# Optimization experiments

Measured on AMD Instinct MI355X. Metric: run time of the kernel, lower is better.

## Reference

```python
import jax, jax.numpy as jnp
import numpy as np

B, T, C = 4, 2048, 768
N_HEADS = 16
HEAD_DIM = C // N_HEADS  # 48
ROPE_BASE = 10000.0


def setup_inputs() -> dict:
    key = jax.random.key(0)
    ks = jax.random.split(key, 6)
    s = 0.02
    return {
        "hidden_states": jax.random.normal(ks[0], (B, T, C), dtype=jnp.float32),
        "attention_mask": jnp.ones((B, T), dtype=jnp.float32),
        "Wq": jax.random.normal(ks[1], (C, C), dtype=jnp.float32) * s,
        "bq": jnp.zeros((C,), dtype=jnp.float32),
        "Wk": jax.random.normal(ks[2], (C, C), dtype=jnp.float32) * s,
        "bk": jnp.zeros((C,), dtype=jnp.float32),
        "Wv": jax.random.normal(ks[3], (C, C), dtype=jnp.float32) * s,
        "bv": jnp.zeros((C,), dtype=jnp.float32),
        "Wo": jax.random.normal(ks[4], (C, C), dtype=jnp.float32) * s,
        "bo": jnp.zeros((C,), dtype=jnp.float32),
    }


def _rotate_half(x):
    x1, x2 = jnp.split(x, 2, axis=-1)
    return jnp.concatenate([-x2, x1], axis=-1)


def reference(hidden_states, attention_mask, Wq, bq, Wk, bk, Wv, bv, Wo, bo):
    b, t, c = hidden_states.shape
    h, d = N_HEADS, c // N_HEADS

    def split_heads(x):  # [b,t,c] -> [b,h,t,d]
        return x.reshape(b, t, h, d).transpose(0, 2, 1, 3)

    q = split_heads(hidden_states @ Wq.T + bq)
    k = split_heads(hidden_states @ Wk.T + bk)
    v = split_heads(hidden_states @ Wv.T + bv)

    # rotary embedding: cos/sin [t, d]
    pos = jnp.arange(t, dtype=jnp.float32)
    inv_freq = 1.0 / (ROPE_BASE ** (jnp.arange(0, d, 2, dtype=jnp.float32) / d))
    freqs = pos[:, None] * inv_freq[None, :]          # [t, d/2]
    emb = jnp.concatenate([freqs, freqs], axis=-1)    # [t, d]
    cos, sin = jnp.cos(emb), jnp.sin(emb)
    q = q * cos + _rotate_half(q) * sin
    k = k * cos + _rotate_half(k) * sin

    scores = jnp.einsum('bhqd,bhkd->bhqk', q, k) / jnp.sqrt(jnp.asarray(d, q.dtype))
    # additive padding mask: (1 - mask) * -10000, broadcast [b,1,1,t]
    scores = scores + (1.0 - attention_mask)[:, None, None, :] * -10000.0
    # causal mask with -inf
    causal = jnp.tril(jnp.ones((t, t), dtype=bool))
    scores = jnp.where(causal[None, None], scores, -jnp.inf)

    probs = jax.nn.softmax(scores, axis=-1)
    ctx = jnp.einsum('bhqk,bhkd->bhqd', probs, v)
    ctx = ctx.transpose(0, 2, 1, 3).reshape(b, t, c)
    return ctx @ Wo.T + bo
```

## Files before the change

kernel.cpp:

```cpp
#include <hip/hip_runtime.h>
#include <hip/hip_bf16.h>
#include <math.h>

#define BB 4
#define TT 2048
#define CC 768
#define NHD 16
#define HD 48
#define NQT 32

typedef __hip_bfloat16 bf16;
typedef __attribute__((ext_vector_type(8))) short short8;
typedef __attribute__((ext_vector_type(4))) float floatx4;

__device__ __forceinline__ unsigned short f2bf(float x) {
    bf16 h = __float2bfloat16(x);
    return *(unsigned short*)&h;
}
__device__ __forceinline__ float bfu2f(unsigned short u) {
    return __uint_as_float(((unsigned)u) << 16);
}

__device__ __forceinline__ void gl_lds16(const void* g, void* s) {
    __builtin_amdgcn_global_load_lds((const __attribute__((address_space(1))) void*)g,
                                     (__attribute__((address_space(3))) void*)s, 16, 0, 0);
}

__device__ __forceinline__ unsigned int pk_bf2(float a, float b) {
    unsigned int ua = __float_as_uint(a) + 0x8000u;
    unsigned int ub = __float_as_uint(b) + 0x8000u;
    return __builtin_amdgcn_perm(ub, ua, 0x07060302);
}

__global__ __launch_bounds__(256) void cast_hs(const float* __restrict__ src,
                                               unsigned short* __restrict__ dst) {
    int i = (blockIdx.x * 256 + threadIdx.x) * 4;
    float4 v = *(const float4*)(src + i);
    ushort4 p;
    p.x = f2bf(v.x); p.y = f2bf(v.y); p.z = f2bf(v.z); p.w = f2bf(v.w);
    *(ushort4*)(dst + i) = p;
}

__global__ __launch_bounds__(256) void cast_w4(const float* __restrict__ s0, const float* __restrict__ s1,
                                               const float* __restrict__ s2, const float* __restrict__ s3,
                                               unsigned short* __restrict__ d0, unsigned short* __restrict__ d1,
                                               unsigned short* __restrict__ d2, unsigned short* __restrict__ d3) {
    const float* s; unsigned short* d;
    switch (blockIdx.y) {
        case 0: s = s0; d = d0; break;
        case 1: s = s1; d = d1; break;
        case 2: s = s2; d = d2; break;
        default: s = s3; d = d3; break;
    }
    int i = (blockIdx.x * 256 + threadIdx.x) * 4;
    float4 v = *(const float4*)(s + i);
    ushort4 p;
    p.x = f2bf(v.x); p.y = f2bf(v.y); p.z = f2bf(v.z); p.w = f2bf(v.w);
    *(ushort4*)(d + i) = p;
}

template <int MODE>
__global__ __launch_bounds__(256) void gemm_mfma(const unsigned short* __restrict__ A,
                                                 const unsigned short* __restrict__ Bw,
                                                 const float* __restrict__ b0p,
                                                 const float* __restrict__ b1p,
                                                 const float* __restrict__ b2p,
                                                 void* __restrict__ out0,
                                                 void* __restrict__ out1,
                                                 void* __restrict__ out2) {
    __shared__ __align__(16) unsigned short As[128][64];
    __shared__ __align__(16) unsigned short Bs[128][64];
    const int tid = threadIdx.x;
    const int w = tid >> 6, lane = tid & 63;
    const int quad = lane >> 4, ln = lane & 15;
    const int wr = w >> 1, wc = w & 1;
    const int n0 = blockIdx.x * 128;
    const int m0 = blockIdx.y * 128;

    const int srow = lane >> 3;
    const int ssw = ((lane & 7) ^ srow) * 8;
    const unsigned short* agp[4];
    const unsigned short* bgp[4];
    void* asl[4];
    void* bsl[4];
#pragma unroll
    for (int i = 0; i < 4; ++i) {
        const int R = i * 32 + w * 8;
        agp[i] = A + (size_t)(m0 + R + srow) * CC + ssw;
        bgp[i] = Bw + (size_t)(n0 + R + srow) * CC + ssw;
        asl[i] = &As[R][0];
        bsl[i] = &Bs[R][0];
    }

    floatx4 acc[4][4];
#pragma unroll
    for (int mi = 0; mi < 4; ++mi)
#pragma unroll
        for (int ni = 0; ni < 4; ++ni) acc[mi][ni] = (floatx4){0.f, 0.f, 0.f, 0.f};

    const int ps0 = (quad ^ (ln & 7)) * 8;

    for (int k0 = 0; k0 < CC; k0 += 64) {
        __syncthreads();
#pragma unroll
        for (int i = 0; i < 4; ++i) {
            gl_lds16(agp[i] + k0, asl[i]);
            gl_lds16(bgp[i] + k0, bsl[i]);
        }
        __syncthreads();
#pragma unroll
        for (int kh = 0; kh < 2; ++kh) {
            const int ps = ps0 ^ (kh * 32);
            short8 af[4], bfr[4];
#pragma unroll
            for (int mi = 0; mi < 4; ++mi)
                af[mi] = *(const short8*)&As[wr * 64 + mi * 16 + ln][ps];
#pragma unroll
            for (int ni = 0; ni < 4; ++ni)
                bfr[ni] = *(const short8*)&Bs[wc * 64 + ni * 16 + ln][ps];
#pragma unroll
            for (int mi = 0; mi < 4; ++mi)
#pragma unroll
                for (int ni = 0; ni < 4; ++ni)
                    acc[mi][ni] = __builtin_amdgcn_mfma_f32_16x16x32_bf16(af[mi], bfr[ni], acc[mi][ni], 0, 0, 0);
        }
    }

    if (MODE == 0) {
        float* outf = (float*)out0;
        float bv[4];
#pragma unroll
        for (int ni = 0; ni < 4; ++ni) bv[ni] = b0p[n0 + wc * 64 + ni * 16 + ln];
#pragma unroll
        for (int mi = 0; mi < 4; ++mi)
#pragma unroll
            for (int r = 0; r < 4; ++r) {
                size_t row = m0 + wr * 64 + mi * 16 + quad * 4 + r;
#pragma unroll
                for (int ni = 0; ni < 4; ++ni)
                    outf[row * CC + n0 + wc * 64 + ni * 16 + ln] = acc[mi][ni][r] + bv[ni];
            }
    } else {
        const int seg = n0 / CC;
        const int nl0 = n0 - seg * CC;
        const float* bp = (seg == 0) ? b0p : (seg == 1) ? b1p : b2p;
        float bv[4];
#pragma unroll
        for (int ni = 0; ni < 4; ++ni) bv[ni] = bp[nl0 + wc * 64 + ni * 16 + ln];

        if (seg < 2) {
            unsigned short* outb = (unsigned short*)(seg == 0 ? out0 : out1);
#pragma unroll
            for (int mi = 0; mi < 4; ++mi)
#pragma unroll
                for (int r = 0; r < 4; ++r) {
                    size_t row = m0 + wr * 64 + mi * 16 + quad * 4 + r;
#pragma unroll
                    for (int ni = 0; ni < 4; ++ni)
                        outb[row * CC + nl0 + wc * 64 + ni * 16 + ln] = f2bf(acc[mi][ni][r] + bv[ni]);
                }
        } else {
            unsigned short* outb = (unsigned short*)out2;
            const int b = m0 >> 11;
#pragma unroll
            for (int ni = 0; ni < 4; ++ni) {
                int col = nl0 + wc * 64 + ni * 16 + ln;
                int h = col / HD, d = col % HD;
                size_t base = (size_t)((b * NHD + h) * HD + d) * TT;
#pragma unroll
                for (int mi = 0; mi < 4; ++mi) {
                    int t = (m0 & 2047) + wr * 64 + mi * 16 + quad * 4;
                    ushort4 pk;
                    pk.x = f2bf(acc[mi][ni][0] + bv[ni]);
                    pk.y = f2bf(acc[mi][ni][1] + bv[ni]);
                    pk.z = f2bf(acc[mi][ni][2] + bv[ni]);
                    pk.w = f2bf(acc[mi][ni][3] + bv[ni]);
                    *(ushort4*)(outb + base + t) = pk;
                }
            }
        }
    }
}

__global__ __launch_bounds__(256) void rope_bf(unsigned short* __restrict__ q,
                                               unsigned short* __restrict__ k) {
    int idx = blockIdx.x * blockDim.x + threadIdx.x;
    const int HALF = HD / 2;
    int p = idx % HALF;
    int rest = idx / HALF;
    int h = rest % NHD;
    int n = rest / NHD;
    int t = n % TT;
    const float QSC = 0.14433756729740643f * 1.4426950408889634f;
    float inv_freq = powf(10000.0f, -((float)(2 * p) / (float)HD));
    float ang = (float)t * inv_freq;
    float sn, cs;
    sincosf(ang, &sn, &cs);
    size_t base = (size_t)n * CC + h * HD + p;
    float x1 = bfu2f(q[base]), x2 = bfu2f(q[base + HALF]);
    q[base] = f2bf((x1 * cs - x2 * sn) * QSC);
    q[base + HALF] = f2bf((x2 * cs + x1 * sn) * QSC);
    x1 = bfu2f(k[base]); x2 = bfu2f(k[base + HALF]);
    k[base] = f2bf(x1 * cs - x2 * sn);
    k[base + HALF] = f2bf(x2 * cs + x1 * sn);
}

__global__ __launch_bounds__(256) void attn_kernel(const unsigned short* __restrict__ qb,
                                                   const unsigned short* __restrict__ kb,
                                                   const unsigned short* __restrict__ vt,
                                                   const float* __restrict__ amask,
                                                   unsigned short* __restrict__ ctx) {
    const int pair = blockIdx.x, h = blockIdx.y, b = blockIdx.z;
    const int tid = threadIdx.x;
    const int w = tid >> 6, lane = tid & 63;
    const int g = lane >> 4, ln = lane & 15;

    __shared__ __align__(16) unsigned short Qs[64][72];
    __shared__ __align__(16) unsigned short Ks[64][72];
    __shared__ __align__(16) unsigned short Vs[64][72];
    __shared__ __align__(16) unsigned short Pw[4][16][72];
    __shared__ __align__(16) float l_s[4][16];

    {
        short8 z8 = {0, 0, 0, 0, 0, 0, 0, 0};
        short8 o8 = {0x3F80, 0, 0, 0, 0, 0, 0, 0};
        short8 ones8 = {0x3F80, 0x3F80, 0x3F80, 0x3F80, 0x3F80, 0x3F80, 0x3F80, 0x3F80};
        if (tid < 128) {
            int r = tid >> 1, half = tid & 1;
            *(short8*)&Qs[r][48 + half * 8] = half ? z8 : o8;
            int t2 = tid;
            *(short8*)&Ks[t2 >> 1][48 + (t2 & 1) * 8] = z8;
        } else if (tid < 128 + 144) {
            int t3 = tid - 128;
            int r = 48 + t3 / 9, cseg = t3 % 9;
            *(short8*)&Vs[r][cseg * 8] = (r == 48) ? ones8 : z8;
        }
    }

    const int ck1 = tid + 256;
    const int rK0 = tid / 6, sK0 = tid % 6;
    const int rK1 = ck1 / 6, sK1 = ck1 % 6;
    const int rV0 = tid >> 3, sV0 = tid & 7;
    const int rV1 = ck1 >> 3, sV1 = ck1 & 7;
    const unsigned short* kbase0 = kb + (size_t)(b * TT + rK0) * CC + h * HD + sK0 * 8;
    const unsigned short* kbase1 = kb + (size_t)(b * TT + rK1) * CC + h * HD + sK1 * 8;
    const unsigned short* vbase0 = vt + (size_t)((b * NHD + h) * HD + rV0) * TT + sV0 * 8;
    const unsigned short* vbase1 = vt + (size_t)((b * NHD + h) * HD + rV1) * TT + sV1 * 8;
    const float* mbase = amask + b * TT + (tid & 63);
    const float MBS = -10000.0f * 1.4426950408889634f;

    for (int rep = 0; rep < 2; ++rep) {
        const int qt = rep ? (NQT - 1 - pair) : pair;
        const int q0 = qt * 64;
        __syncthreads();
        *(short8*)&Qs[rK0][sK0 * 8] =
            *(const short8*)(qb + (size_t)(b * TT + q0 + rK0) * CC + h * HD + sK0 * 8);
        if (tid < 128)
            *(short8*)&Qs[rK1][sK1 * 8] =
                *(const short8*)(qb + (size_t)(b * TT + q0 + rK1) * CC + h * HD + sK1 * 8);

        const unsigned short* kp0 = kbase0;
        const unsigned short* kp1 = kbase1;
        const unsigned short* vp0 = vbase0;
        const unsigned short* vp1 = vbase1;
        const float* mp = mbase;
        short8 kr0, kr1, vr0, vr1;
        float mr = 1.0f;
        kr0 = *(const short8*)kp0;
        vr0 = *(const short8*)vp0;
        if (tid < 128) { kr1 = *(const short8*)kp1; vr1 = *(const short8*)vp1; }
        if (tid < 64) mr = *mp;
        __syncthreads();

        short8 aq0 = *(const short8*)&Qs[w * 16 + ln][g * 8];
        short8 aq1 = *(const short8*)&Qs[w * 16 + ln][32 + g * 8];
        const int q_lane = q0 + w * 16 + ln;

        floatx4 o0 = {0.f, 0.f, 0.f, 0.f}, o1 = o0, o2 = o0, o3 = o0;

        for (int kt = 0; kt <= qt; ++kt) {
            __syncthreads();
            *(short8*)&Ks[rK0][sK0 * 8] = kr0;
            *(short8*)&Vs[rV0][sV0 * 8] = vr0;
            if (tid < 128) {
                *(short8*)&Ks[rK1][sK1 * 8] = kr1;
                *(short8*)&Vs[rV1][sV1 * 8] = vr1;
            }
            if (tid < 64) Ks[tid][48] = f2bf((1.0f - mr) * MBS);
            __syncthreads();

            if (kt < qt) {
                kp0 += (size_t)64 * CC; kr0 = *(const short8*)kp0;
                vp0 += 64;              vr0 = *(const short8*)vp0;
                if (tid < 128) {
                    kp1 += (size_t)64 * CC; kr1 = *(const short8*)kp1;
                    vp1 += 64;              vr1 = *(const short8*)vp1;
                }
                if (tid < 64) { mp += 64; mr = *mp; }
            }

            const int k0 = kt * 64;
            floatx4 sc[4];
#pragma unroll
            for (int c = 0; c < 4; ++c) {
                short8 kf0 = *(const short8*)&Ks[c * 16 + ln][g * 8];
                short8 kf1 = *(const short8*)&Ks[c * 16 + ln][32 + g * 8];
                floatx4 z = {0.f, 0.f, 0.f, 0.f};
                z = __builtin_amdgcn_mfma_f32_16x16x32_bf16(kf0, aq0, z, 0, 0, 0);
                z = __builtin_amdgcn_mfma_f32_16x16x32_bf16(kf1, aq1, z, 0, 0, 0);
                sc[c] = z;
            }

            const bool diag = (kt == qt);
#pragma unroll
            for (int c = 0; c < 4; ++c) {
                float pv[4];
#pragma unroll
                for (int r = 0; r < 4; ++r) {
                    float e = __builtin_amdgcn_exp2f(sc[c][r]);
                    if (diag && (k0 + c * 16 + g * 4 + r > q_lane)) e = 0.f;
                    pv[r] = e;
                }
                uint2 pk;
                pk.x = pk_bf2(pv[0], pv[1]);
                pk.y = pk_bf2(pv[2], pv[3]);
                *(uint2*)&Pw[w][ln][c * 16 + g * 4] = pk;
            }
            short8 pa0 = *(const short8*)&Pw[w][ln][g * 8];
            short8 pa1 = *(const short8*)&Pw[w][ln][32 + g * 8];
#pragma unroll
            for (int n = 0; n < 4; ++n) {
                short8 vb0 = *(const short8*)&Vs[n * 16 + ln][g * 8];
                short8 vb1 = *(const short8*)&Vs[n * 16 + ln][32 + g * 8];
                floatx4 acc = (n == 0) ? o0 : (n == 1) ? o1 : (n == 2) ? o2 : o3;
                acc = __builtin_amdgcn_mfma_f32_16x16x32_bf16(pa0, vb0, acc, 0, 0, 0);
                acc = __builtin_amdgcn_mfma_f32_16x16x32_bf16(pa1, vb1, acc, 0, 0, 0);
                if (n == 0) o0 = acc; else if (n == 1) o1 = acc; else if (n == 2) o2 = acc; else o3 = acc;
            }
        }

        if (ln == 0) *(floatx4*)&l_s[w][g * 4] = o3;
        floatx4 l4 = *(const floatx4*)&l_s[w][g * 4];
#pragma unroll
        for (int r = 0; r < 4; ++r) {
            float inv_l = 1.0f / l4[r];
            int t = q0 + w * 16 + g * 4 + r;
            unsigned short* dst = ctx + (size_t)(b * TT + t) * CC + h * HD;
            dst[ln] = f2bf(o0[r] * inv_l);
            dst[16 + ln] = f2bf(o1[r] * inv_l);
            dst[32 + ln] = f2bf(o2[r] * inv_l);
        }
    }
}

extern "C" void kernel_launch(void* const* d_in, const int* in_sizes, int n_in,
                              void* d_out, int out_size, void* d_ws, size_t ws_size,
                              hipStream_t stream) {
    const float* hs = (const float*)d_in[0];
    const float* amask = (const float*)d_in[1];
    const float* Wq = (const float*)d_in[2];
    const float* bq = (const float*)d_in[3];
    const float* Wk = (const float*)d_in[4];
    const float* bk = (const float*)d_in[5];
    const float* Wv = (const float*)d_in[6];
    const float* bv = (const float*)d_in[7];
    const float* Wo = (const float*)d_in[8];
    const float* bo = (const float*)d_in[9];

    const size_t NELEM = (size_t)BB * TT * CC;
    const size_t WELEM = (size_t)CC * CC;
    unsigned short* hb  = (unsigned short*)d_ws;
    unsigned short* qbuf = hb + NELEM;
    unsigned short* kbuf = qbuf + NELEM;
    unsigned short* vtb = kbuf + NELEM;
    unsigned short* ctxb = vtb + NELEM;
    unsigned short* wqb = ctxb + NELEM;
    unsigned short* wkb = wqb + WELEM;
    unsigned short* wvb = wkb + WELEM;
    unsigned short* wob = wvb + WELEM;

    cast_hs<<<NELEM / 1024, 256, 0, stream>>>(hs, hb);
    dim3 wgrid(WELEM / 1024, 4);
    cast_w4<<<wgrid, 256, 0, stream>>>(Wq, Wk, Wv, Wo, wqb, wkb, wvb, wob);

    dim3 qkvgrid(3 * CC / 128, (BB * TT) / 128);
    gemm_mfma<1><<<qkvgrid, 256, 0, stream>>>(hb, wqb, bq, bk, bv, qbuf, kbuf, vtb);

    int rope_total = BB * TT * NHD * (HD / 2);
    rope_bf<<<rope_total / 256, 256, 0, stream>>>(qbuf, kbuf);

    dim3 agrid(NQT / 2, NHD, BB);
    attn_kernel<<<agrid, 256, 0, stream>>>(qbuf, kbuf, vtb, amask, ctxb);

    dim3 ogrid(CC / 128, (BB * TT) / 128);
    gemm_mfma<0><<<ogrid, 256, 0, stream>>>(ctxb, wob, bo, nullptr, nullptr,
                                            (float*)d_out, nullptr, nullptr);
}
```

Baseline: 250.3 us.

## Remap block indices for XCD locality and precompute RoPE sin/cos table

Flattens the GEMM and attention grids to 1D and remaps block IDs so that blocks landing on the same XCD (round-robin by blockIdx mod 8) share the same M rows or the same (batch, head). This is meant to improve per-XCD L2 reuse of A tiles and of K/V. Separately, RoPE sin/cos values are precomputed once into a small table in the workspace instead of calling powf and sincosf per element. The table adds an extra tiny kernel launch and relies on workspace space past the weight buffers.

```diff
diff --git a/kernel.cpp b/kernel.cpp
--- a/kernel.cpp
+++ b/kernel.cpp
@@ -57,6 +57,16 @@
     ushort4 p;
     p.x = f2bf(v.x); p.y = f2bf(v.y); p.z = f2bf(v.z); p.w = f2bf(v.w);
     *(ushort4*)(d + i) = p;
+}
+
+__global__ __launch_bounds__(256) void rope_table(float2* __restrict__ tab) {
+    int idx = blockIdx.x * 256 + threadIdx.x;
+    int t = idx / 24, p = idx % 24;
+    float inv_freq = powf(10000.0f, -((float)(2 * p) / (float)HD));
+    float ang = (float)t * inv_freq;
+    float sn, cs;
+    sincosf(ang, &sn, &cs);
+    tab[idx] = make_float2(cs, sn);
 }
 
 template <int MODE>
@@ -74,8 +84,12 @@
     const int w = tid >> 6, lane = tid & 63;
     const int quad = lane >> 4, ln = lane & 15;
     const int wr = w >> 1, wc = w & 1;
-    const int n0 = blockIdx.x * 128;
-    const int m0 = blockIdx.y * 128;
+
+    const int NXB = (MODE == 1) ? 18 : 6;
+    const int bx = blockIdx.x;
+    const int xcd = bx & 7, slot = bx >> 3;
+    const int n0 = (slot % NXB) * 128;
+    const int m0 = ((slot / NXB) * 8 + xcd) * 128;
 
     const int srow = lane >> 3;
     const int ssw = ((lane & 7) ^ srow) * 8;
@@ -183,7 +197,8 @@
 }
 
 __global__ __launch_bounds__(256) void rope_bf(unsigned short* __restrict__ q,
-                                               unsigned short* __restrict__ k) {
+                                               unsigned short* __restrict__ k,
+                                               const float2* __restrict__ tab) {
     int idx = blockIdx.x * blockDim.x + threadIdx.x;
     const int HALF = HD / 2;
     int p = idx % HALF;
@@ -192,10 +207,8 @@
     int n = rest / NHD;
     int t = n % TT;
     const float QSC = 0.14433756729740643f * 1.4426950408889634f;
-    float inv_freq = powf(10000.0f, -((float)(2 * p) / (float)HD));
-    float ang = (float)t * inv_freq;
-    float sn, cs;
-    sincosf(ang, &sn, &cs);
+    float2 cssn = tab[t * HALF + p];
+    float cs = cssn.x, sn = cssn.y;
     size_t base = (size_t)n * CC + h * HD + p;
     float x1 = bfu2f(q[base]), x2 = bfu2f(q[base + HALF]);
     q[base] = f2bf((x1 * cs - x2 * sn) * QSC);
@@ -210,7 +223,12 @@
                                                    const unsigned short* __restrict__ vt,
                                                    const float* __restrict__ amask,
                                                    unsigned short* __restrict__ ctx) {
-    const int pair = blockIdx.x, h = blockIdx.y, b = blockIdx.z;
+    const int bx = blockIdx.x;
+    const int xcd = bx & 7;
+    const int rem = bx >> 3;
+    const int pair = rem & 15;
+    const int j = ((rem >> 4) << 3) | xcd;
+    const int b = j >> 4, h = j & 15;
     const int tid = threadIdx.x;
     const int w = tid >> 6, lane = tid & 63;
     const int g = lane >> 4, ln = lane & 15;
@@ -378,21 +396,20 @@
     unsigned short* wkb = wqb + WELEM;
     unsigned short* wvb = wkb + WELEM;
     unsigned short* wob = wvb + WELEM;
+    float2* ropetab = (float2*)(wob + WELEM);
 
     cast_hs<<<NELEM / 1024, 256, 0, stream>>>(hs, hb);
     dim3 wgrid(WELEM / 1024, 4);
     cast_w4<<<wgrid, 256, 0, stream>>>(Wq, Wk, Wv, Wo, wqb, wkb, wvb, wob);
-
-    dim3 qkvgrid(3 * CC / 128, (BB * TT) / 128);
-    gemm_mfma<1><<<qkvgrid, 256, 0, stream>>>(hb, wqb, bq, bk, bv, qbuf, kbuf, vtb);
+    rope_table<<<(TT * (HD / 2)) / 256, 256, 0, stream>>>(ropetab);
+
+    gemm_mfma<1><<<18 * 64, 256, 0, stream>>>(hb, wqb, bq, bk, bv, qbuf, kbuf, vtb);
 
     int rope_total = BB * TT * NHD * (HD / 2);
-    rope_bf<<<rope_total / 256, 256, 0, stream>>>(qbuf, kbuf);
-
-    dim3 agrid(NQT / 2, NHD, BB);
-    attn_kernel<<<agrid, 256, 0, stream>>>(qbuf, kbuf, vtb, amask, ctxb);
-
-    dim3 ogrid(CC / 128, (BB * TT) / 128);
-    gemm_mfma<0><<<ogrid, 256, 0, stream>>>(ctxb, wob, bo, nullptr, nullptr,
-                                            (float*)d_out, nullptr, nullptr);
-}
+    rope_bf<<<rope_total / 256, 256, 0, stream>>>(qbuf, kbuf, ropetab);
+
+    attn_kernel<<<1024, 256, 0, stream>>>(qbuf, kbuf, vtb, amask, ctxb);
+
+    gemm_mfma<0><<<6 * 64, 256, 0, stream>>>(ctxb, wob, bo, nullptr, nullptr,
+                                             (float*)d_out, nullptr, nullptr);
+}
```

Measured after the change: 233.1 us. -6.9%, faster.
